# Optimization experiments

Hardware: AMD Instinct MI355X
Metric: run time of the kernel (lower is better)

## Reference

```python
import jax, jax.numpy as jnp
import numpy as np

N, IN_DIM, LAT, NB = 4096, 3000, 64, 2
SINKHORN_ITERS = 3


def _bce_logits(x, y):
    # torch BCEWithLogitsLoss, mean reduction, numerically stable
    return jnp.mean(jnp.maximum(x, 0.0) - x * y + jnp.log1p(jnp.exp(-jnp.abs(x))))


def _forward(feature_set, adj_set, graph_neigh_set, label_CSL_set, dist_mat_set,
             enc_W, dec_W, Ms, disc_W, disc_b, perm_idx):
    nb = feature_set.shape[0]
    hs = []
    loss_sl = 0.0
    loss_feat = 0.0
    for k in range(nb):  # small fixed loop over slices
        x, adj, mask, lab = feature_set[k], adj_set[k], graph_neigh_set[k], label_CSL_set[k]
        h = adj @ (x @ enc_W[k])            # GCN encode: spmm(adj, x @ W)
        out = adj @ (h @ dec_W[k])          # GCN decode
        x_a = x[perm_idx[k]]                # permutation(x): row shuffle
        h_a = adj @ (x_a @ enc_W[k])
        hr, har = jax.nn.relu(h), jax.nn.relu(h_a)

        def readout(emb):
            vsum = mask @ emb
            ge = vsum / mask.sum(1, keepdims=True)
            nrm = jnp.linalg.norm(ge, axis=1, keepdims=True)
            return ge / jnp.maximum(nrm, 1e-12)   # F.normalize p=2

        g = jax.nn.sigmoid(readout(hr))
        g_a = jax.nn.sigmoid(readout(har))

        def disc(c, hp, hm):
            s1 = jnp.einsum('nd,de,ne->n', hp, disc_W, c) + disc_b[0]
            s2 = jnp.einsum('nd,de,ne->n', hm, disc_W, c) + disc_b[0]
            return jnp.stack([s1, s2], axis=1)  # [N,2]

        ret = disc(g, hr, har)
        ret_a = disc(g_a, har, hr)
        loss_sl = loss_sl + _bce_logits(ret, lab) + _bce_logits(ret_a, lab)
        loss_feat = loss_feat + jnp.mean((x - out) ** 2)
        hs.append(h)

    loss_align = 0.0; loss_align_fix = 0.0; loss_maintain = 0.0
    loss_marginal = 0.0; loss_sparsity = 0.0
    for k in range(1, nb):
        src, tgt = hs[k - 1], hs[k]
        M = Ms[k - 1]
        m1, m2 = src.shape[0], tgt.shape[0]
        C = (src @ M) @ (tgt @ M).T / jnp.sqrt(jnp.float32(M.shape[0]))
        P = jax.nn.softmax(C, axis=1) / m1
        # NonSquareSinkhornKnopp.fit: alternate row/col normalization to uniform marginals
        for _ in range(SINKHORN_ITERS):
            P = P / (m1 * P.sum(1, keepdims=True))
            P = P / (m2 * P.sum(0, keepdims=True))
        cxy = P / P.sum(1, keepdims=True)
        cyx = P.T / P.T.sum(1, keepdims=True)
        # cdist(src, tgt)
        d2 = jnp.sum(src ** 2, 1)[:, None] + jnp.sum(tgt ** 2, 1)[None, :] - 2.0 * (src @ tgt.T)
        cd = jnp.sqrt(jnp.maximum(d2, 1e-12))
        loss_align = loss_align + jnp.sum(P * cd)
        f0, f1 = feature_set[k - 1], feature_set[k]
        loss_align_fix = loss_align_fix + jnp.mean((f0 - cxy @ f1) ** 2) + jnp.mean((f1 - cyx @ f0) ** 2)
        D0, D1 = dist_mat_set[k - 1], dist_mat_set[k]
        diff1 = D0 - cxy @ (D1 @ cxy.T)
        diff2 = D1 - cyx @ (D0 @ cyx.T)
        loss_maintain = loss_maintain + jnp.linalg.norm(diff1) / m1 + jnp.linalg.norm(diff2) / m2
        # replicate torch F.kl_div(input, target) = mean(target*(log target - input))
        p = jnp.full((m2,), 1.0 / m2, jnp.float32)
        q = P.sum(0)
        kld_pq = jnp.mean(q * (jnp.log(q) - p))
        kld_pp = jnp.mean(p * (jnp.log(p) - p))
        loss_marginal = loss_marginal + (kld_pq - kld_pp) * m2
        loss_sparsity = loss_sparsity - jnp.sum(P * jnp.log(P + 1e-10))
    return jnp.stack([loss_sl, loss_feat, loss_align, loss_align_fix,
                      loss_maintain, loss_marginal, loss_sparsity])


def setup_inputs():
    key = jax.random.key(0)
    ks = jax.random.split(key, 12)
    feature_set = jax.random.normal(ks[0], (NB, N, IN_DIM), jnp.float32)
    A = jax.random.uniform(ks[1], (NB, N, N), jnp.float32)
    adj_set = A / A.sum(-1, keepdims=True)  # row-stochastic dense stand-in for normalized sparse adj
    mask = (jax.random.uniform(ks[2], (NB, N, N)) < 0.01).astype(jnp.float32)
    graph_neigh_set = mask + jnp.eye(N, dtype=jnp.float32)[None]  # nonzero row sums
    lab = jnp.concatenate([jnp.ones((N, 1)), jnp.zeros((N, 1))], axis=1).astype(jnp.float32)
    label_CSL_set = jnp.broadcast_to(lab, (NB, N, 2))
    D = jax.random.uniform(ks[3], (NB, N, N), jnp.float32)
    dist_mat_set = 0.5 * (D + jnp.swapaxes(D, 1, 2))
    perm_idx = jnp.stack([jax.random.permutation(ks[4 + i], N) for i in range(NB)]).astype(jnp.int32)
    s_enc = np.float32(np.sqrt(2.0 / (IN_DIM + LAT)))
    enc_W = jax.random.normal(ks[6], (NB, IN_DIM, LAT), jnp.float32) * s_enc
    dec_W = jax.random.normal(ks[7], (NB, LAT, IN_DIM), jnp.float32) * s_enc
    s_lat = np.float32(np.sqrt(1.0 / LAT))
    Ms = jax.random.normal(ks[8], (NB - 1, LAT, LAT), jnp.float32) * s_lat
    disc_W = jax.random.normal(ks[9], (LAT, LAT), jnp.float32) * s_lat
    disc_b = jnp.zeros((1,), jnp.float32)
    return dict(feature_set=feature_set, adj_set=adj_set, graph_neigh_set=graph_neigh_set,
                label_CSL_set=label_CSL_set, dist_mat_set=dist_mat_set, perm_idx=perm_idx,
                enc_W=enc_W, dec_W=dec_W, Ms=Ms, disc_W=disc_W, disc_b=disc_b)


def reference(feature_set, adj_set, graph_neigh_set, label_CSL_set, dist_mat_set,
              perm_idx, enc_W, dec_W, Ms, disc_W, disc_b):
    return _forward(feature_set, adj_set, graph_neigh_set, label_CSL_set, dist_mat_set,
                    enc_W, dec_W, Ms, disc_W, disc_b, perm_idx)
```

## Files before the change

kernel.cpp:

```cpp
#include <hip/hip_runtime.h>
#include <cmath>

constexpr int kN   = 4096;
constexpr int kIN  = 3000;
constexpr int kINp = 3072;
constexpr int kLAT = 64;

enum { SL = 0, FEAT, ALN, FXA, FXB, SM1, SM2, SPS, NSLOT };

typedef __bf16 bf16x8 __attribute__((ext_vector_type(8)));
typedef float f32x4 __attribute__((ext_vector_type(4)));
typedef unsigned short u16x8 __attribute__((ext_vector_type(8)));
typedef unsigned short u16x4 __attribute__((ext_vector_type(4)));

template<bool IS_MAX>
__device__ __forceinline__ float blk_red(float v) {
  __shared__ float buf[8];
  #pragma unroll
  for (int s = 32; s > 0; s >>= 1) {
    float o = __shfl_down(v, s, 64);
    v = IS_MAX ? fmaxf(v, o) : (v + o);
  }
  int lane = threadIdx.x & 63, wv = threadIdx.x >> 6, nw = blockDim.x >> 6;
  __syncthreads();
  if (lane == 0) buf[wv] = v;
  __syncthreads();
  float r = buf[0];
  for (int i = 1; i < nw; i++) r = IS_MAX ? fmaxf(r, buf[i]) : (r + buf[i]);
  return r;
}

__device__ __forceinline__ float wave_red_sum(float v) {
  #pragma unroll
  for (int s = 32; s > 0; s >>= 1) v += __shfl_down(v, s, 64);
  return v;
}

__device__ __forceinline__ unsigned short f2bf(float f) {
  unsigned u = __builtin_bit_cast(unsigned, f);
  u += 0x7fffu + ((u >> 16) & 1u);
  return (unsigned short)(u >> 16);
}
__device__ __forceinline__ float bf2f(unsigned short h) {
  return __builtin_bit_cast(float, (unsigned)h << 16);
}

__device__ __forceinline__ void gload16(const unsigned short* g, unsigned short* l) {
  __builtin_amdgcn_global_load_lds(
      (const __attribute__((address_space(1))) unsigned int*)g,
      (__attribute__((address_space(3))) unsigned int*)l, 16, 0, 0);
}

#define VMW(n) asm volatile("s_waitcnt vmcnt(" #n ")" ::: "memory")

template<int EPI, int XBF>
__global__ __launch_bounds__(256)
void bt_mfma_k(const unsigned short* __restrict__ A, const unsigned short* __restrict__ Bt,
               unsigned short* __restrict__ Cb, float* __restrict__ Cf,
               const void* __restrict__ Xv,
               const float* __restrict__ rowdiv, const float* __restrict__ coldiv,
               float* __restrict__ slot, int gx, int Nc, int K, int ldX, int sym)
{
  __shared__ unsigned short AB[3 * 8192];

  int orig = blockIdx.x;
  int bx, by;
  if (EPI == 2 && sym) {
    int x = orig & 7, i = orig >> 3;
    int u = x * 66 + i;
    float disc = 4225.f - 8.f * (float)u;
    by = (int)((65.f - sqrtf(fmaxf(disc, 0.f))) * 0.5f);
    while (by > 0 && 32 * by - by * (by - 1) / 2 > u) by--;
    while (32 * (by + 1) - (by + 1) * by / 2 <= u) by++;
    bx = by + (u - (32 * by - by * (by - 1) / 2));
  } else {
    int x = orig & 7, tt = orig >> 3;
    bx = tt >> 2;
    by = x * 4 + (tt & 3);
  }
  const int row0 = by * 128, col0 = bx * 128;

  const int t = threadIdx.x, l = t & 63, wv = t >> 6;
  const int wr = wv >> 1, wc = wv & 1;
  const int lr = l & 15, lkh = (l >> 4) << 3;

  f32x4 acc[4][4];
  #pragma unroll
  for (int i = 0; i < 4; i++)
    #pragma unroll
    for (int j = 0; j < 4; j++) acc[i][j] = (f32x4){0.f, 0.f, 0.f, 0.f};

  const int srow = l >> 2;
  const int sk   = (l & 3) << 3;
  const unsigned short* Ab = A  + (size_t)(row0 + srow) * K + sk;
  const unsigned short* Bb = Bt + (size_t)(col0 + srow) * K + sk;

  const int NT = K >> 5;

  auto STAGE = [&](int kt, int buf) {
    unsigned short* As = AB + buf * 8192;
    unsigned short* Bs = As + 4096;
    int k0 = kt << 5;
    #pragma unroll
    for (int h2 = 0; h2 < 2; h2++) {
      int c = wv * 2 + h2;
      gload16(Ab + (size_t)c * 16 * K + k0, As + c * 512);
      gload16(Bb + (size_t)c * 16 * K + k0, Bs + c * 512);
    }
  };

  STAGE(0, 0);
  if (NT > 1) STAGE(1, 1);
  if (NT > 2) STAGE(2, 2);
  int cur = 0;

  for (int kt = 0; kt < NT; ++kt) {
    int ahead = NT - 1 - kt;
    if (ahead >= 2)      { VMW(8); }
    else if (ahead == 1) { VMW(4); }
    else                 { VMW(0); }
    __builtin_amdgcn_sched_barrier(0);
    __builtin_amdgcn_s_barrier();

    const unsigned short* As = AB + cur * 8192;
    const unsigned short* Bs = As + 4096;
    u16x8 af[4], bfv[4];
    #pragma unroll
    for (int mi = 0; mi < 4; mi++)
      af[mi] = *(const u16x8*)&As[(wr * 64 + mi * 16 + lr) * 32 + lkh];
    #pragma unroll
    for (int ni = 0; ni < 4; ni++)
      bfv[ni] = *(const u16x8*)&Bs[(wc * 64 + ni * 16 + lr) * 32 + lkh];
    #pragma unroll
    for (int mi = 0; mi < 4; mi++)
      #pragma unroll
      for (int ni = 0; ni < 4; ni++)
        acc[mi][ni] = __builtin_amdgcn_mfma_f32_16x16x32_bf16(
            __builtin_bit_cast(bf16x8, af[mi]),
            __builtin_bit_cast(bf16x8, bfv[ni]), acc[mi][ni], 0, 0, 0);

    __builtin_amdgcn_s_barrier();
    if (kt + 3 < NT) STAGE(kt + 3, cur);
    cur = (cur == 2) ? 0 : cur + 1;
  }

  const int lcol = l & 15, lrow = (l >> 4) << 2;
  if (EPI == 0) {
    #pragma unroll
    for (int mi = 0; mi < 4; mi++) {
      int rr = row0 + wr * 64 + mi * 16 + lrow;
      #pragma unroll
      for (int ni = 0; ni < 4; ni++) {
        int cc = col0 + wc * 64 + ni * 16 + lcol;
        #pragma unroll
        for (int r = 0; r < 4; r++) {
          float v = acc[mi][ni][r];
          if (rowdiv) v /= rowdiv[rr + r];
          Cb[(size_t)(rr + r) * 4096 + cc] = f2bf(v);
        }
      }
    }
  } else if (EPI == 1) {
    #pragma unroll
    for (int mi = 0; mi < 4; mi++) {
      int rr = row0 + wr * 64 + mi * 16 + lrow;
      #pragma unroll
      for (int ni = 0; ni < 4; ni++) {
        int cc = col0 + wc * 64 + ni * 16 + lcol;
        #pragma unroll
        for (int r = 0; r < 4; r++)
          Cf[(size_t)(rr + r) * 4096 + cc] = acc[mi][ni][r];
      }
    }
  } else if (EPI == 2) {
    const float* Xf = (const float*)Xv;
    const unsigned short* Xh = (const unsigned short*)Xv;
    float part = 0.f;
    #pragma unroll
    for (int mi = 0; mi < 4; mi++) {
      int rr = row0 + wr * 64 + mi * 16 + lrow;
      #pragma unroll
      for (int ni = 0; ni < 4; ni++) {
        int cc = col0 + wc * 64 + ni * 16 + lcol;
        if (cc < Nc) {
          float cd = coldiv ? coldiv[cc] : 1.f;
          #pragma unroll
          for (int r = 0; r < 4; r++) {
            float v = acc[mi][ni][r];
            if (rowdiv) v /= rowdiv[rr + r];
            v /= cd;
            size_t xi = (size_t)(rr + r) * ldX + cc;
            float xval = XBF ? bf2f(Xh[xi]) : Xf[xi];
            float d = xval - v;
            part = fmaf(d, d, part);
          }
        }
      }
    }
    part = blk_red<false>(part);
    if (t == 0) {
      float wgt = (sym && col0 > row0) ? 2.f : 1.f;
      atomicAdd(slot, part * wgt);
    }
  } else {
    const unsigned short* Ph = (const unsigned short*)Xv;
    float a = 0.f, sp = 0.f;
    #pragma unroll
    for (int mi = 0; mi < 4; mi++) {
      int rr = row0 + wr * 64 + mi * 16 + lrow;
      #pragma unroll
      for (int ni = 0; ni < 4; ni++) {
        int cc = col0 + wc * 64 + ni * 16 + lcol;
        #pragma unroll
        for (int r = 0; r < 4; r++) {
          float g = acc[mi][ni][r];
          float p = bf2f(Ph[(size_t)(rr + r) * ldX + cc]);
          float d2 = rowdiv[rr + r] + coldiv[cc] - 2.f * g;
          a = fmaf(p, sqrtf(fmaxf(d2, 1e-12f)), a);
          sp = fmaf(p, logf(p + 1e-10f), sp);
        }
      }
    }
    a = blk_red<false>(a);
    sp = blk_red<false>(sp);
    if (t == 0) { atomicAdd(&slot[ALN], a); atomicAdd(&slot[SPS], sp); }
  }
}

__global__ __launch_bounds__(256)
void ns_mfma_k(const unsigned short* __restrict__ A, const unsigned short* __restrict__ Bt,
               float* __restrict__ C, int Nc, int K, int KC, int ldC)
{
  __shared__ unsigned short AB[2 * 8192];
  int ks = blockIdx.x & 15, strip = blockIdx.x >> 4;
  const int row0 = strip * 128;
  const int kbase = ks * KC;

  const int t = threadIdx.x, l = t & 63, wv = t >> 6;
  const int wr = wv >> 1, wc = wv & 1;
  const int lr = l & 15, lkh = (l >> 4) << 3;

  f32x4 acc[4][4];
  #pragma unroll
  for (int i = 0; i < 4; i++)
    #pragma unroll
    for (int j = 0; j < 4; j++) acc[i][j] = (f32x4){0.f, 0.f, 0.f, 0.f};

  const int srow = l >> 2;
  const int sk   = (l & 3) << 3;
  const unsigned short* Ab = A  + (size_t)(row0 + srow) * K + kbase + sk;
  const unsigned short* Bb = Bt + (size_t)srow * K + kbase + sk;

  const int NT = KC >> 5;

  auto STAGE = [&](int kt, int buf) {
    unsigned short* As = AB + buf * 8192;
    unsigned short* Bs = As + 4096;
    int k0 = kt << 5;
    #pragma unroll
    for (int h2 = 0; h2 < 2; h2++) {
      int c = wv * 2 + h2;
      gload16(Ab + (size_t)c * 16 * K + k0, As + c * 512);
      gload16(Bb + (size_t)c * 16 * K + k0, Bs + c * 512);
    }
  };

  STAGE(0, 0);
  if (NT > 1) STAGE(1, 1);
  int cur = 0;

  for (int kt = 0; kt < NT; ++kt) {
    if (kt + 1 < NT) { VMW(4); }
    else             { VMW(0); }
    __builtin_amdgcn_sched_barrier(0);
    __builtin_amdgcn_s_barrier();

    const unsigned short* As = AB + cur * 8192;
    const unsigned short* Bs = As + 4096;
    u16x8 af[4], bfv[4];
    #pragma unroll
    for (int mi = 0; mi < 4; mi++)
      af[mi] = *(const u16x8*)&As[(wr * 64 + mi * 16 + lr) * 32 + lkh];
    #pragma unroll
    for (int ni = 0; ni < 4; ni++)
      bfv[ni] = *(const u16x8*)&Bs[(wc * 64 + ni * 16 + lr) * 32 + lkh];
    #pragma unroll
    for (int mi = 0; mi < 4; mi++)
      #pragma unroll
      for (int ni = 0; ni < 4; ni++)
        acc[mi][ni] = __builtin_amdgcn_mfma_f32_16x16x32_bf16(
            __builtin_bit_cast(bf16x8, af[mi]),
            __builtin_bit_cast(bf16x8, bfv[ni]), acc[mi][ni], 0, 0, 0);

    __builtin_amdgcn_s_barrier();
    if (kt + 2 < NT) STAGE(kt + 2, cur);
    cur ^= 1;
  }

  const int lcol = l & 15, lrow = (l >> 4) << 2;
  #pragma unroll
  for (int mi = 0; mi < 4; mi++) {
    int rr = row0 + wr * 64 + mi * 16 + lrow;
    #pragma unroll
    for (int ni = 0; ni < 4; ni++) {
      int cc = wc * 64 + ni * 16 + lcol;
      if (cc < Nc) {
        #pragma unroll
        for (int r = 0; r < 4; r++)
          atomicAdd(&C[(size_t)(rr + r) * ldC + cc], acc[mi][ni][r]);
      }
    }
  }
}

__global__ void cvt_k(const float* __restrict__ s, unsigned short* __restrict__ d,
                      int n8, float scale)
{
  int i = blockIdx.x * 256 + threadIdx.x;
  if (i < n8) {
    float4 a = ((const float4*)s)[2 * i], b = ((const float4*)s)[2 * i + 1];
    u16x8 w;
    w[0] = f2bf(a.x * scale); w[1] = f2bf(a.y * scale);
    w[2] = f2bf(a.z * scale); w[3] = f2bf(a.w * scale);
    w[4] = f2bf(b.x * scale); w[5] = f2bf(b.y * scale);
    w[6] = f2bf(b.z * scale); w[7] = f2bf(b.w * scale);
    ((u16x8*)d)[i] = w;
  }
}

__global__ void cvt_rs_k(const float* __restrict__ s, unsigned short* __restrict__ d,
                         float* __restrict__ mrs)
{
  int i = blockIdx.x * 256 + threadIdx.x;
  float4 a = ((const float4*)s)[2 * i], b = ((const float4*)s)[2 * i + 1];
  u16x8 w;
  w[0] = f2bf(a.x); w[1] = f2bf(a.y); w[2] = f2bf(a.z); w[3] = f2bf(a.w);
  w[4] = f2bf(b.x); w[5] = f2bf(b.y); w[6] = f2bf(b.z); w[7] = f2bf(b.w);
  ((u16x8*)d)[i] = w;
  float s8 = a.x + a.y + a.z + a.w + b.x + b.y + b.z + b.w;
  float ws = wave_red_sum(s8);
  if ((threadIdx.x & 63) == 0) atomicAdd(&mrs[i >> 9], ws);
}

__global__ void cvt_pad_k(const float* __restrict__ s, unsigned short* __restrict__ d)
{
  int i = blockIdx.x * 256 + threadIdx.x;
  int row = i / 384, c8 = (i - row * 384) * 8;
  u16x8 w = (u16x8)0;
  if (c8 < kIN) {
    const float* sp = s + (size_t)row * kIN + c8;
    float4 a = *(const float4*)sp, b = *(const float4*)(sp + 4);
    w[0] = f2bf(a.x); w[1] = f2bf(a.y); w[2] = f2bf(a.z); w[3] = f2bf(a.w);
    w[4] = f2bf(b.x); w[5] = f2bf(b.y); w[6] = f2bf(b.z); w[7] = f2bf(b.w);
  }
  ((u16x8*)d)[i] = w;
}

__global__ void cvtsq_k(const float* __restrict__ H, unsigned short* __restrict__ hb,
                        float* __restrict__ outv)
{
  int row = blockIdx.x * 4 + (threadIdx.x >> 6), j = threadIdx.x & 63;
  float v = H[(size_t)row * 128 + j];
  hb[(size_t)row * 64 + j] = f2bf(v);
  float p = wave_red_sum(v * v);
  if (j == 0) outv[row] = p;
}

template<bool RELU>
__global__ void tr_k(const float* __restrict__ src, unsigned short* __restrict__ dst,
                     int R, int C, int sld, int dld)
{
  __shared__ float tile[32][33];
  int c0 = blockIdx.x * 32, r0 = blockIdx.y * 32;
  int tr_ = threadIdx.x >> 3, tc4 = (threadIdx.x & 7) << 2;
  #pragma unroll
  for (int j = 0; j < 4; j++) {
    int r = r0 + tr_, c = c0 + tc4 + j;
    float v = (r < R && c < C) ? src[(size_t)r * sld + c] : 0.f;
    if (RELU) v = fmaxf(v, 0.f);
    tile[tr_][tc4 + j] = v;
  }
  __syncthreads();
  u16x4 wv;
  #pragma unroll
  for (int j = 0; j < 4; j++) wv[j] = f2bf(tile[tc4 + j][tr_]);
  *(u16x4*)&dst[(size_t)(c0 + tr_) * dld + r0 + tc4] = wv;
}

__global__ void tr_bf_k(const unsigned short* __restrict__ src,
                        unsigned short* __restrict__ dst, int R, int C)
{
  __shared__ unsigned short tile[32][36];
  int c0 = blockIdx.x * 32, r0 = blockIdx.y * 32;
  int tr_ = threadIdx.x >> 3, tc4 = (threadIdx.x & 7) << 2;
  *(u16x4*)&tile[tr_][tc4] = *(const u16x4*)&src[(size_t)(r0 + tr_) * C + c0 + tc4];
  __syncthreads();
  u16x4 w;
  #pragma unroll
  for (int j = 0; j < 4; j++) w[j] = tile[tc4 + j][tr_];
  *(u16x4*)&dst[(size_t)(c0 + tr_) * R + r0 + tc4] = w;
}

template<bool RELU>
__global__ __launch_bounds__(256)
void gemm_small_k(const float* __restrict__ A, const float* __restrict__ B,
                  float* __restrict__ C, int M, int Nc, int K,
                  int ldA, int ldB, int ldC)
{
  __shared__ float As[16][68];
  __shared__ float Bs[16][68];
  int tid = threadIdx.x;
  int tx = tid & 15, ty = tid >> 4;
  int row0 = blockIdx.y * 64, col0 = blockIdx.x * 64;
  float acc[4][4] = {};

  for (int k0 = 0; k0 < K; k0 += 16) {
    {
      int m = tid >> 2, kk = (tid & 3) << 2;
      const float* ap = A + (size_t)(row0 + m) * ldA + k0 + kk;
      float4 v = *(const float4*)ap;
      if (RELU) {
        v.x = fmaxf(v.x, 0.f); v.y = fmaxf(v.y, 0.f);
        v.z = fmaxf(v.z, 0.f); v.w = fmaxf(v.w, 0.f);
      }
      As[kk + 0][m] = v.x; As[kk + 1][m] = v.y; As[kk + 2][m] = v.z; As[kk + 3][m] = v.w;
    }
    {
      int kk = tid >> 4, c = (tid & 15) << 2;
      const float* bp = B + (size_t)(k0 + kk) * ldB + col0 + c;
      #pragma unroll
      for (int i = 0; i < 4; i++)
        Bs[kk][c + i] = (col0 + c + i < Nc) ? bp[i] : 0.f;
    }
    __syncthreads();
    #pragma unroll
    for (int kk = 0; kk < 16; kk++) {
      float4 a4 = *(const float4*)&As[kk][ty << 2];
      float4 b4 = *(const float4*)&Bs[kk][tx << 2];
      float av[4] = {a4.x, a4.y, a4.z, a4.w};
      float bv[4] = {b4.x, b4.y, b4.z, b4.w};
      #pragma unroll
      for (int i = 0; i < 4; i++)
        #pragma unroll
        for (int j = 0; j < 4; j++)
          acc[i][j] = fmaf(av[i], bv[j], acc[i][j]);
    }
    __syncthreads();
  }
  #pragma unroll
  for (int i = 0; i < 4; i++) {
    int r = row0 + (ty << 2) + i;
    #pragma unroll
    for (int j = 0; j < 4; j++) {
      int c = col0 + (tx << 2) + j;
      if (c < Nc) C[(size_t)r * ldC + c] = acc[i][j];
    }
  }
}

__global__ __launch_bounds__(256)
void sink_k(float* __restrict__ P, unsigned short* __restrict__ Pb,
            const float* __restrict__ cs_in, float* __restrict__ cs_out,
            float* __restrict__ rs, int mode)
{
  int tid = threadIdx.x;
  int r0 = blockIdx.x * 8;
  float csl[16] = {};
  float cdiv[16];
  if (mode != 0) {
    #pragma unroll
    for (int t = 0; t < 4; t++) {
      float4 c4 = ((const float4*)cs_in)[tid + t * 256];
      cdiv[4 * t + 0] = 1.f / (4096.f * c4.x);
      cdiv[4 * t + 1] = 1.f / (4096.f * c4.y);
      cdiv[4 * t + 2] = 1.f / (4096.f * c4.z);
      cdiv[4 * t + 3] = 1.f / (4096.f * c4.w);
    }
  }
  for (int rr = 0; rr < 8; rr++) {
    int row = r0 + rr;
    float4* prow = (float4*)(P + (size_t)row * 4096);
    float4 r[4];
    #pragma unroll
    for (int t = 0; t < 4; t++) r[t] = prow[tid + t * 256];

    if (mode == 0) {
      float m = -3.4e38f;
      #pragma unroll
      for (int t = 0; t < 4; t++)
        m = fmaxf(m, fmaxf(fmaxf(r[t].x, r[t].y), fmaxf(r[t].z, r[t].w)));
      m = blk_red<true>(m);
      float s = 0.f;
      #pragma unroll
      for (int t = 0; t < 4; t++) {
        r[t].x = expf(r[t].x - m); r[t].y = expf(r[t].y - m);
        r[t].z = expf(r[t].z - m); r[t].w = expf(r[t].w - m);
        s += r[t].x + r[t].y + r[t].z + r[t].w;
      }
      s = blk_red<false>(s);
      float f = 1.f / (s * 4096.f);
      #pragma unroll
      for (int t = 0; t < 4; t++) {
        r[t].x *= f; r[t].y *= f; r[t].z *= f; r[t].w *= f;
        prow[tid + t * 256] = r[t];
        csl[4 * t + 0] += r[t].x; csl[4 * t + 1] += r[t].y;
        csl[4 * t + 2] += r[t].z; csl[4 * t + 3] += r[t].w;
      }
    } else {
      float s = 0.f;
      #pragma unroll
      for (int t = 0; t < 4; t++) {
        r[t].x *= cdiv[4 * t + 0]; r[t].y *= cdiv[4 * t + 1];
        r[t].z *= cdiv[4 * t + 2]; r[t].w *= cdiv[4 * t + 3];
        s += r[t].x + r[t].y + r[t].z + r[t].w;
      }
      s = blk_red<false>(s);
      if (mode == 1) {
        float f = 1.f / (4096.f * s);
        #pragma unroll
        for (int t = 0; t < 4; t++) {
          r[t].x *= f; r[t].y *= f; r[t].z *= f; r[t].w *= f;
          prow[tid + t * 256] = r[t];
          csl[4 * t + 0] += r[t].x; csl[4 * t + 1] += r[t].y;
          csl[4 * t + 2] += r[t].z; csl[4 * t + 3] += r[t].w;
        }
      } else {
        if (tid == 0) rs[row] = s;
        #pragma unroll
        for (int t = 0; t < 4; t++) {
          prow[tid + t * 256] = r[t];
          u16x4 w;
          w[0] = f2bf(r[t].x); w[1] = f2bf(r[t].y);
          w[2] = f2bf(r[t].z); w[3] = f2bf(r[t].w);
          *(u16x4*)&Pb[(size_t)row * 4096 + 4 * (tid + t * 256)] = w;
          csl[4 * t + 0] += r[t].x; csl[4 * t + 1] += r[t].y;
          csl[4 * t + 2] += r[t].z; csl[4 * t + 3] += r[t].w;
        }
      }
    }
  }
  #pragma unroll
  for (int t = 0; t < 4; t++) {
    int j = 4 * (tid + t * 256);
    atomicAdd(&cs_out[j + 0], csl[4 * t + 0]);
    atomicAdd(&cs_out[j + 1], csl[4 * t + 1]);
    atomicAdd(&cs_out[j + 2], csl[4 * t + 2]);
    atomicAdd(&cs_out[j + 3], csl[4 * t + 3]);
  }
}

__global__ void gather_k(float* __restrict__ XP, const int* __restrict__ perm)
{
  int gid = blockIdx.x * 256 + threadIdx.x;
  int i = gid >> 6, j = gid & 63;
  XP[(size_t)i * 128 + 64 + j] = XP[(size_t)perm[i] * 128 + j];
}

__global__ void readout_k(const float* __restrict__ vs2, const float* __restrict__ mrs,
                          float* __restrict__ g2)
{
  int q = blockIdx.x, j = threadIdx.x;
  float v = vs2[(size_t)q * 64 + j] / mrs[q >> 1];
  float p = v * v;
  #pragma unroll
  for (int s = 1; s < 64; s <<= 1) p += __shfl_xor(p, s, 64);
  float nrm = sqrtf(p);
  v = v / fmaxf(nrm, 1e-12f);
  g2[(size_t)q * 64 + j] = 1.f / (1.f + expf(-v));
}

__device__ __forceinline__ float bce_term(float x, float y) {
  return fmaxf(x, 0.f) - x * y + log1pf(expf(-fabsf(x)));
}

__global__ void disc_k(const float* __restrict__ G2, const float* __restrict__ W2,
                       const float* __restrict__ lab, const float* __restrict__ bptr,
                       float* __restrict__ acc)
{
  int i = blockIdx.x, j = threadIdx.x;
  float gj  = G2[(size_t)(2 * i) * 64 + j];
  float gaj = G2[(size_t)(2 * i + 1) * 64 + j];
  float hw  = W2[(size_t)(2 * i) * 64 + j];
  float haw = W2[(size_t)(2 * i + 1) * 64 + j];
  float s1 = hw * gj, s2 = haw * gj, s1a = haw * gaj, s2a = hw * gaj;
  #pragma unroll
  for (int s = 1; s < 64; s <<= 1) {
    s1  += __shfl_xor(s1, s, 64);
    s2  += __shfl_xor(s2, s, 64);
    s1a += __shfl_xor(s1a, s, 64);
    s2a += __shfl_xor(s2a, s, 64);
  }
  if (j == 0) {
    float b = bptr[0];
    float y0 = lab[i * 2 + 0], y1 = lab[i * 2 + 1];
    float t = bce_term(s1 + b, y0) + bce_term(s2 + b, y1)
            + bce_term(s1a + b, y0) + bce_term(s2a + b, y1);
    atomicAdd(&acc[SL], t);
  }
}

__global__ __launch_bounds__(256)
void finalize_k(const float* __restrict__ acc, const float* __restrict__ cs,
                float* __restrict__ out)
{
  int tid = threadIdx.x;
  float invm2 = 1.f / (float)kN;
  float t = 0.f;
  for (int j = tid; j < kN; j += 256) {
    float q = cs[j];
    t += q * (logf(q) - invm2);
  }
  t = blk_red<false>(t);
  if (tid == 0) {
    float kld_pq = t * invm2;
    float kld_pp = invm2 * (logf(invm2) - invm2);
    out[0] = acc[SL] / (2.f * (float)kN);
    out[1] = acc[FEAT] / ((float)kN * (float)kIN);
    out[2] = acc[ALN];
    out[3] = (acc[FXA] + acc[FXB]) / ((float)kN * (float)kIN);
    out[4] = sqrtf(acc[SM1]) / (float)kN + sqrtf(acc[SM2]) / (float)kN;
    out[5] = (kld_pq - kld_pp) * (float)kN;
    out[6] = -acc[SPS];
  }
}

extern "C" void kernel_launch(void* const* d_in, const int* in_sizes, int n_in,
                              void* d_out, int out_size, void* d_ws, size_t ws_size,
                              hipStream_t stream)
{
  (void)in_sizes; (void)n_in; (void)out_size; (void)ws_size;
  const float* feat  = (const float*)d_in[0];
  const float* adjs  = (const float*)d_in[1];
  const float* gmask = (const float*)d_in[2];
  const float* labs  = (const float*)d_in[3];
  const float* dists = (const float*)d_in[4];
  const int*   perms = (const int*)d_in[5];
  const float* encW  = (const float*)d_in[6];
  const float* decW  = (const float*)d_in[7];
  const float* MsW   = (const float*)d_in[8];
  const float* discW = (const float*)d_in[9];
  const float* discb = (const float*)d_in[10];
  float* out = (float*)d_out;

  const size_t SZNN = (size_t)kN * kN;

  char* cur = (char*)d_ws;
  auto alloc = [&](size_t bytes) {
    char* p = cur;
    cur += (bytes + 255) & ~(size_t)255;
    return p;
  };
  float* P            = (float*)alloc(SZNN * 4);
  unsigned short* Pb  = (unsigned short*)alloc(SZNN * 2);
  unsigned short* PbT = (unsigned short*)alloc(SZNN * 2);
  unsigned short* Db  = (unsigned short*)alloc(SZNN * 2);
  unsigned short* ajb = (unsigned short*)alloc(SZNN * 2);
  unsigned short* xb0 = (unsigned short*)alloc((size_t)kN * kINp * 2);
  unsigned short* xb1 = (unsigned short*)alloc((size_t)kN * kINp * 2);
  unsigned short* dWtb= (unsigned short*)alloc((size_t)kINp * kLAT * 2);
  unsigned short* ahb = (unsigned short*)alloc((size_t)kN * kLAT * 2);
  unsigned short* encWtp = (unsigned short*)alloc((size_t)128 * kINp * 2);
  unsigned short* XPt = (unsigned short*)alloc((size_t)128 * kN * 2);
  unsigned short* hbTp= (unsigned short*)alloc((size_t)128 * kN * 2);
  unsigned short* HRt = (unsigned short*)alloc((size_t)128 * kN * 2);
  unsigned short* smb = (unsigned short*)alloc((size_t)kN * kLAT * 2);
  unsigned short* tmb = (unsigned short*)alloc((size_t)kN * kLAT * 2);
  unsigned short* h0b = (unsigned short*)alloc((size_t)kN * kLAT * 2);
  unsigned short* h1b = (unsigned short*)alloc((size_t)kN * kLAT * 2);
  float* XP  = (float*)alloc((size_t)kN * 128 * 4);
  float* HH0 = (float*)alloc((size_t)kN * 128 * 4);
  float* HH1 = (float*)alloc((size_t)kN * 128 * 4);
  float* VS  = (float*)alloc((size_t)kN * 128 * 4);
  float* G2  = (float*)alloc((size_t)kN * 128 * 4);
  float* W2  = (float*)alloc((size_t)kN * 128 * 4);
  float* SM_ = (float*)alloc((size_t)kN * kLAT * 4);
  float* TM_ = (float*)alloc((size_t)kN * kLAT * 4);
  float* ah  = (float*)alloc((size_t)kN * kLAT * 4);
  float* sns = (float*)alloc(kN * 4);
  float* snt = (float*)alloc(kN * 4);
  float* rs  = (float*)alloc(kN * 4);
  float* cs  = (float*)alloc(kN * 4);
  float* csA = (float*)alloc(kN * 4);
  float* csB = (float*)alloc(kN * 4);
  float* mrs = (float*)alloc(kN * 4);
  float* acc = (float*)alloc(NSLOT * 4);

  unsigned short* Tb  = (unsigned short*)P;
  unsigned short* ftb = ajb;

  hipMemsetAsync(acc, 0, NSLOT * sizeof(float), stream);

  for (int k = 0; k < 2; k++) {
    const float* x    = feat  + (size_t)k * kN * kIN;
    const float* adj  = adjs  + (size_t)k * SZNN;
    const float* msk  = gmask + (size_t)k * SZNN;
    const float* lab  = labs  + (size_t)k * kN * 2;
    const int*   perm = perms + (size_t)k * kN;
    const float* eW   = encW  + (size_t)k * kIN * kLAT;
    const float* dW   = decW  + (size_t)k * kLAT * kIN;
    float* HHk = (k == 0) ? HH0 : HH1;
    unsigned short* xbk = (k == 0) ? xb0 : xb1;

    cvt_pad_k<<<6144, 256, 0, stream>>>(x, xbk);
    hipMemsetAsync(encWtp, 0, (size_t)128 * kINp * 2, stream);
    tr_k<false><<<dim3(2, (kIN + 31) / 32), 256, 0, stream>>>(eW, encWtp, kIN, kLAT, kLAT, kINp);
    hipMemsetAsync(XP, 0, (size_t)kN * 128 * 4, stream);
    ns_mfma_k<<<512, 256, 0, stream>>>(xbk, encWtp, XP, kLAT, kINp, kINp / 16, 128);
    gather_k<<<kN * 64 / 256, 256, 0, stream>>>(XP, perm);
    tr_k<false><<<dim3(4, 128), 256, 0, stream>>>(XP, XPt, kN, 128, 128, kN);
    cvt_k<<<(int)(SZNN / 8 / 256), 256, 0, stream>>>(adj, ajb, (int)(SZNN / 8), 1.f);
    hipMemsetAsync(HHk, 0, (size_t)kN * 128 * 4, stream);
    ns_mfma_k<<<512, 256, 0, stream>>>(ajb, XPt, HHk, 128, kN, kN / 16, 128);
    hipMemsetAsync(hbTp, 0, (size_t)128 * kN * 2, stream);
    tr_k<false><<<dim3(2, 128), 256, 0, stream>>>(HHk, hbTp, kN, kLAT, 128, kN);
    hipMemsetAsync(ah, 0, (size_t)kN * kLAT * 4, stream);
    ns_mfma_k<<<512, 256, 0, stream>>>(ajb, hbTp, ah, kLAT, kN, kN / 16, kLAT);
    cvt_k<<<128, 256, 0, stream>>>(ah, ahb, kN * kLAT / 8, 1.f);
    tr_k<false><<<dim3(kINp / 32, 2), 256, 0, stream>>>(dW, dWtb, kLAT, kIN, kIN, kLAT);
    bt_mfma_k<2, 1><<<(kINp / 128) * 32, 256, 0, stream>>>(
        ahb, dWtb, nullptr, nullptr, xbk, nullptr, nullptr, &acc[FEAT],
        kINp / 128, kIN, kLAT, kINp, 0);
    tr_k<true><<<dim3(4, 128), 256, 0, stream>>>(HHk, HRt, kN, 128, 128, kN);
    hipMemsetAsync(mrs, 0, kN * 4, stream);
    cvt_rs_k<<<(int)(SZNN / 8 / 256), 256, 0, stream>>>(msk, ajb, mrs);
    hipMemsetAsync(VS, 0, (size_t)kN * 128 * 4, stream);
    ns_mfma_k<<<512, 256, 0, stream>>>(ajb, HRt, VS, 128, kN, kN / 16, 128);
    readout_k<<<2 * kN, 64, 0, stream>>>(VS, mrs, G2);
    gemm_small_k<true><<<dim3(1, 128), 256, 0, stream>>>(HHk, discW, W2, 2 * kN, kLAT,
                                                         kLAT, kLAT, kLAT, kLAT);
    disc_k<<<kN, 64, 0, stream>>>(G2, W2, lab, discb, acc);
  }

  const float* D0 = dists;
  const float* D1 = dists + SZNN;

  gemm_small_k<false><<<dim3(1, 64), 256, 0, stream>>>(HH0, MsW, SM_, kN, kLAT, kLAT,
                                                       128, kLAT, kLAT);
  gemm_small_k<false><<<dim3(1, 64), 256, 0, stream>>>(HH1, MsW, TM_, kN, kLAT, kLAT,
                                                       128, kLAT, kLAT);
  cvt_k<<<128, 256, 0, stream>>>(SM_, smb, kN * kLAT / 8, 0.125f);
  cvt_k<<<128, 256, 0, stream>>>(TM_, tmb, kN * kLAT / 8, 1.f);
  bt_mfma_k<1, 0><<<1024, 256, 0, stream>>>(smb, tmb, nullptr, P, nullptr, nullptr, nullptr,
                                            nullptr, 32, kN, kLAT, 0, 0);

  hipMemsetAsync(csA, 0, kN * 4, stream);
  sink_k<<<512, 256, 0, stream>>>(P, nullptr, nullptr, csA, nullptr, 0);
  hipMemsetAsync(csB, 0, kN * 4, stream);
  sink_k<<<512, 256, 0, stream>>>(P, nullptr, csA, csB, nullptr, 1);
  hipMemsetAsync(csA, 0, kN * 4, stream);
  sink_k<<<512, 256, 0, stream>>>(P, nullptr, csB, csA, nullptr, 1);
  hipMemsetAsync(cs, 0, kN * 4, stream);
  sink_k<<<512, 256, 0, stream>>>(P, Pb, csA, cs, rs, 2);

  tr_k<false><<<dim3(kN / 32, kN / 32), 256, 0, stream>>>(P, PbT, kN, kN, kN, kN);

  cvtsq_k<<<1024, 256, 0, stream>>>(HH0, h0b, sns);
  cvtsq_k<<<1024, 256, 0, stream>>>(HH1, h1b, snt);
  bt_mfma_k<3, 1><<<1024, 256, 0, stream>>>(h0b, h1b, nullptr, nullptr, Pb, sns, snt, acc,
                                            32, kN, kLAT, kN, 0);

  tr_bf_k<<<dim3(kINp / 32, kN / 32), 256, 0, stream>>>(xb1, ftb, kN, kINp);
  bt_mfma_k<2, 1><<<(kINp / 128) * 32, 256, 0, stream>>>(
      Pb, ftb, nullptr, nullptr, xb0, rs, nullptr, &acc[FXA], kINp / 128, kIN, kN, kINp, 0);
  tr_bf_k<<<dim3(kINp / 32, kN / 32), 256, 0, stream>>>(xb0, ftb, kN, kINp);
  bt_mfma_k<2, 1><<<(kINp / 128) * 32, 256, 0, stream>>>(
      PbT, ftb, nullptr, nullptr, xb1, cs, nullptr, &acc[FXB], kINp / 128, kIN, kN, kINp, 0);

  cvt_k<<<(int)(SZNN / 8 / 256), 256, 0, stream>>>(D1, Db, (int)(SZNN / 8), 1.f);
  bt_mfma_k<0, 0><<<1024, 256, 0, stream>>>(Pb, Db, Tb, nullptr, nullptr, rs, nullptr,
                                            nullptr, 32, kN, kN, 0, 0);
  bt_mfma_k<2, 0><<<528, 256, 0, stream>>>(Tb, Pb, nullptr, nullptr, D0, nullptr, rs,
                                           &acc[SM1], 32, kN, kN, kN, 1);
  cvt_k<<<(int)(SZNN / 8 / 256), 256, 0, stream>>>(D0, Db, (int)(SZNN / 8), 1.f);
  bt_mfma_k<0, 0><<<1024, 256, 0, stream>>>(PbT, Db, Tb, nullptr, nullptr, cs, nullptr,
                                            nullptr, 32, kN, kN, 0, 0);
  bt_mfma_k<2, 0><<<528, 256, 0, stream>>>(Tb, PbT, nullptr, nullptr, D1, nullptr, cs,
                                           &acc[SM2], 32, kN, kN, kN, 1);

  finalize_k<<<1, 256, 0, stream>>>(acc, cs, out);
}
```

Before: 1.981 ms.

## Merge paired GEMM+reduction launches into one persistent grid-stride kernel

Adds a bt2_mfma_k kernel that runs the tiles of two independent GEMMs with a squared-error epilogue in one launch, using a grid-stride loop over the combined tile list. The two feature-transport GEMMs and the two symmetric smoothness GEMMs are each merged this way. Separate scratch buffers (ftb2, Tb2) let both operands stay live at once. The goal is to fill the GPU better and cut launch and tail gaps, paid for with extra buffer reuse of ajb/Db and a trailing barrier in blk_red.

```diff
diff --git a/kernel.cpp b/kernel.cpp
--- a/kernel.cpp
+++ b/kernel.cpp
@@ -27,6 +27,7 @@
   __syncthreads();
   float r = buf[0];
   for (int i = 1; i < nw; i++) r = IS_MAX ? fmaxf(r, buf[i]) : (r + buf[i]);
+  __syncthreads();
   return r;
 }
 
@@ -52,6 +53,16 @@
 }
 
 #define VMW(n) asm volatile("s_waitcnt vmcnt(" #n ")" ::: "memory")
+
+__device__ __forceinline__ void tri_decode(int lu, int& bx, int& by) {
+  int x = lu & 7, i = lu >> 3;
+  int u = x * 66 + i;
+  float disc = 4225.f - 8.f * (float)u;
+  by = (int)((65.f - sqrtf(fmaxf(disc, 0.f))) * 0.5f);
+  while (by > 0 && 32 * by - by * (by - 1) / 2 > u) by--;
+  while (32 * (by + 1) - (by + 1) * by / 2 <= u) by++;
+  bx = by + (u - (32 * by - by * (by - 1) / 2));
+}
 
 template<int EPI, int XBF>
 __global__ __launch_bounds__(256)
@@ -59,25 +70,14 @@
                unsigned short* __restrict__ Cb, float* __restrict__ Cf,
                const void* __restrict__ Xv,
                const float* __restrict__ rowdiv, const float* __restrict__ coldiv,
-               float* __restrict__ slot, int gx, int Nc, int K, int ldX, int sym)
+               float* __restrict__ slot, int gx, int Nc, int K, int ldX)
 {
   __shared__ unsigned short AB[3 * 8192];
 
   int orig = blockIdx.x;
-  int bx, by;
-  if (EPI == 2 && sym) {
-    int x = orig & 7, i = orig >> 3;
-    int u = x * 66 + i;
-    float disc = 4225.f - 8.f * (float)u;
-    by = (int)((65.f - sqrtf(fmaxf(disc, 0.f))) * 0.5f);
-    while (by > 0 && 32 * by - by * (by - 1) / 2 > u) by--;
-    while (32 * (by + 1) - (by + 1) * by / 2 <= u) by++;
-    bx = by + (u - (32 * by - by * (by - 1) / 2));
-  } else {
-    int x = orig & 7, tt = orig >> 3;
-    bx = tt >> 2;
-    by = x * 4 + (tt & 3);
-  }
+  int x = orig & 7, tt = orig >> 3;
+  int bx = tt >> 2;
+  int by = x * 4 + (tt & 3);
   const int row0 = by * 128, col0 = bx * 128;
 
   const int t = threadIdx.x, l = t & 63, wv = t >> 6;
@@ -198,10 +198,7 @@
       }
     }
     part = blk_red<false>(part);
-    if (t == 0) {
-      float wgt = (sym && col0 > row0) ? 2.f : 1.f;
-      atomicAdd(slot, part * wgt);
-    }
+    if (t == 0) atomicAdd(slot, part);
   } else {
     const unsigned short* Ph = (const unsigned short*)Xv;
     float a = 0.f, sp = 0.f;
@@ -224,6 +221,134 @@
     a = blk_red<false>(a);
     sp = blk_red<false>(sp);
     if (t == 0) { atomicAdd(&slot[ALN], a); atomicAdd(&slot[SPS], sp); }
+  }
+}
+
+template<int XBF, int SYM>
+__global__ __launch_bounds__(256)
+void bt2_mfma_k(const unsigned short* __restrict__ A0, const unsigned short* __restrict__ B0,
+                const void* __restrict__ X0, const float* __restrict__ rd0,
+                const float* __restrict__ cd0, float* __restrict__ slot0,
+                const unsigned short* __restrict__ A1, const unsigned short* __restrict__ B1,
+                const void* __restrict__ X1, const float* __restrict__ rd1,
+                const float* __restrict__ cd1, float* __restrict__ slot1,
+                int gx, int Nc, int K, int ldX, int ntiles, int split)
+{
+  __shared__ unsigned short AB[3 * 8192];
+  const int t = threadIdx.x, l = t & 63, wv = t >> 6;
+  const int wr = wv >> 1, wc = wv & 1;
+  const int lr = l & 15, lkh = (l >> 4) << 3;
+  const int srow = l >> 2;
+  const int sk   = (l & 3) << 3;
+  const int NT = K >> 5;
+
+  for (int u = blockIdx.x; u < ntiles; u += gridDim.x) {
+    const int s1 = (u >= split);
+    const int lu = s1 ? (u - split) : u;
+    const unsigned short* A  = s1 ? A1 : A0;
+    const unsigned short* Bt = s1 ? B1 : B0;
+    const void* Xv           = s1 ? X1 : X0;
+    const float* rowdiv      = s1 ? rd1 : rd0;
+    const float* coldiv      = s1 ? cd1 : cd0;
+    float* slot              = s1 ? slot1 : slot0;
+
+    int bx, by;
+    if (SYM) {
+      tri_decode(lu, bx, by);
+    } else {
+      int x = lu & 7, tt = lu >> 3;
+      bx = tt >> 2;
+      by = x * 4 + (tt & 3);
+    }
+    const int row0 = by * 128, col0 = bx * 128;
+
+    f32x4 acc[4][4];
+    #pragma unroll
+    for (int i = 0; i < 4; i++)
+      #pragma unroll
+      for (int j = 0; j < 4; j++) acc[i][j] = (f32x4){0.f, 0.f, 0.f, 0.f};
+
+    const unsigned short* Ab = A  + (size_t)(row0 + srow) * K + sk;
+    const unsigned short* Bb = Bt + (size_t)(col0 + srow) * K + sk;
+
+    auto STAGE = [&](int kt, int buf) {
+      unsigned short* As = AB + buf * 8192;
+      unsigned short* Bs = As + 4096;
+      int k0 = kt << 5;
+      #pragma unroll
+      for (int h2 = 0; h2 < 2; h2++) {
+        int c = wv * 2 + h2;
+        gload16(Ab + (size_t)c * 16 * K + k0, As + c * 512);
+        gload16(Bb + (size_t)c * 16 * K + k0, Bs + c * 512);
+      }
+    };
+
+    STAGE(0, 0);
+    if (NT > 1) STAGE(1, 1);
+    if (NT > 2) STAGE(2, 2);
+    int cur = 0;
+
+    for (int kt = 0; kt < NT; ++kt) {
+      int ahead = NT - 1 - kt;
+      if (ahead >= 2)      { VMW(8); }
+      else if (ahead == 1) { VMW(4); }
+      else                 { VMW(0); }
+      __builtin_amdgcn_sched_barrier(0);
+      __builtin_amdgcn_s_barrier();
+
+      const unsigned short* As = AB + cur * 8192;
+      const unsigned short* Bs = As + 4096;
+      u16x8 af[4], bfv[4];
+      #pragma unroll
+      for (int mi = 0; mi < 4; mi++)
+        af[mi] = *(const u16x8*)&As[(wr * 64 + mi * 16 + lr) * 32 + lkh];
+      #pragma unroll
+      for (int ni = 0; ni < 4; ni++)
+        bfv[ni] = *(const u16x8*)&Bs[(wc * 64 + ni * 16 + lr) * 32 + lkh];
+      #pragma unroll
+      for (int mi = 0; mi < 4; mi++)
+        #pragma unroll
+        for (int ni = 0; ni < 4; ni++)
+          acc[mi][ni] = __builtin_amdgcn_mfma_f32_16x16x32_bf16(
+              __builtin_bit_cast(bf16x8, af[mi]),
+              __builtin_bit_cast(bf16x8, bfv[ni]), acc[mi][ni], 0, 0, 0);
+
+      __builtin_amdgcn_s_barrier();
+      if (kt + 3 < NT) STAGE(kt + 3, cur);
+      cur = (cur == 2) ? 0 : cur + 1;
+    }
+
+    const int lcol = l & 15, lrow = (l >> 4) << 2;
+    const float* Xf = (const float*)Xv;
+    const unsigned short* Xh = (const unsigned short*)Xv;
+    float part = 0.f;
+    #pragma unroll
+    for (int mi = 0; mi < 4; mi++) {
+      int rr = row0 + wr * 64 + mi * 16 + lrow;
+      #pragma unroll
+      for (int ni = 0; ni < 4; ni++) {
+        int cc = col0 + wc * 64 + ni * 16 + lcol;
+        if (cc < Nc) {
+          float cd = coldiv ? coldiv[cc] : 1.f;
+          #pragma unroll
+          for (int r = 0; r < 4; r++) {
+            float v = acc[mi][ni][r];
+            if (rowdiv) v /= rowdiv[rr + r];
+            v /= cd;
+            size_t xi = (size_t)(rr + r) * ldX + cc;
+            float xval = XBF ? bf2f(Xh[xi]) : Xf[xi];
+            float d = xval - v;
+            part = fmaf(d, d, part);
+          }
+        }
+      }
+    }
+    part = blk_red<false>(part);
+    if (t == 0) {
+      float wgt = (SYM && col0 > row0) ? 2.f : 1.f;
+      atomicAdd(slot, part * wgt);
+    }
+    __syncthreads();
   }
 }
 
@@ -685,8 +810,10 @@
   float* mrs = (float*)alloc(kN * 4);
   float* acc = (float*)alloc(NSLOT * 4);
 
-  unsigned short* Tb  = (unsigned short*)P;
+  unsigned short* Tb1 = (unsigned short*)P;
   unsigned short* ftb = ajb;
+  unsigned short* ftb2= Db;
+  unsigned short* Tb2 = ajb;
 
   hipMemsetAsync(acc, 0, NSLOT * sizeof(float), stream);
 
@@ -719,7 +846,7 @@
     tr_k<false><<<dim3(kINp / 32, 2), 256, 0, stream>>>(dW, dWtb, kLAT, kIN, kIN, kLAT);
     bt_mfma_k<2, 1><<<(kINp / 128) * 32, 256, 0, stream>>>(
         ahb, dWtb, nullptr, nullptr, xbk, nullptr, nullptr, &acc[FEAT],
-        kINp / 128, kIN, kLAT, kINp, 0);
+        kINp / 128, kIN, kLAT, kINp);
     tr_k<true><<<dim3(4, 128), 256, 0, stream>>>(HHk, HRt, kN, 128, 128, kN);
     hipMemsetAsync(mrs, 0, kN * 4, stream);
     cvt_rs_k<<<(int)(SZNN / 8 / 256), 256, 0, stream>>>(msk, ajb, mrs);
@@ -741,7 +868,7 @@
   cvt_k<<<128, 256, 0, stream>>>(SM_, smb, kN * kLAT / 8, 0.125f);
   cvt_k<<<128, 256, 0, stream>>>(TM_, tmb, kN * kLAT / 8, 1.f);
   bt_mfma_k<1, 0><<<1024, 256, 0, stream>>>(smb, tmb, nullptr, P, nullptr, nullptr, nullptr,
-                                            nullptr, 32, kN, kLAT, 0, 0);
+                                            nullptr, 32, kN, kLAT, 0);
 
   hipMemsetAsync(csA, 0, kN * 4, stream);
   sink_k<<<512, 256, 0, stream>>>(P, nullptr, nullptr, csA, nullptr, 0);
@@ -757,25 +884,25 @@
   cvtsq_k<<<1024, 256, 0, stream>>>(HH0, h0b, sns);
   cvtsq_k<<<1024, 256, 0, stream>>>(HH1, h1b, snt);
   bt_mfma_k<3, 1><<<1024, 256, 0, stream>>>(h0b, h1b, nullptr, nullptr, Pb, sns, snt, acc,
-                                            32, kN, kLAT, kN, 0);
+                                            32, kN, kLAT, kN);
 
   tr_bf_k<<<dim3(kINp / 32, kN / 32), 256, 0, stream>>>(xb1, ftb, kN, kINp);
-  bt_mfma_k<2, 1><<<(kINp / 128) * 32, 256, 0, stream>>>(
-      Pb, ftb, nullptr, nullptr, xb0, rs, nullptr, &acc[FXA], kINp / 128, kIN, kN, kINp, 0);
-  tr_bf_k<<<dim3(kINp / 32, kN / 32), 256, 0, stream>>>(xb0, ftb, kN, kINp);
-  bt_mfma_k<2, 1><<<(kINp / 128) * 32, 256, 0, stream>>>(
-      PbT, ftb, nullptr, nullptr, xb1, cs, nullptr, &acc[FXB], kINp / 128, kIN, kN, kINp, 0);
+  tr_bf_k<<<dim3(kINp / 32, kN / 32), 256, 0, stream>>>(xb0, ftb2, kN, kINp);
+  bt2_mfma_k<1, 0><<<1024, 256, 0, stream>>>(
+      Pb,  ftb,  xb0, rs, nullptr, &acc[FXA],
+      PbT, ftb2, xb1, cs, nullptr, &acc[FXB],
+      kINp / 128, kIN, kN, kINp, 2 * (kINp / 128) * 32, (kINp / 128) * 32);
 
   cvt_k<<<(int)(SZNN / 8 / 256), 256, 0, stream>>>(D1, Db, (int)(SZNN / 8), 1.f);
-  bt_mfma_k<0, 0><<<1024, 256, 0, stream>>>(Pb, Db, Tb, nullptr, nullptr, rs, nullptr,
-                                            nullptr, 32, kN, kN, 0, 0);
-  bt_mfma_k<2, 0><<<528, 256, 0, stream>>>(Tb, Pb, nullptr, nullptr, D0, nullptr, rs,
-                                           &acc[SM1], 32, kN, kN, kN, 1);
+  bt_mfma_k<0, 0><<<1024, 256, 0, stream>>>(Pb, Db, Tb1, nullptr, nullptr, rs, nullptr,
+                                            nullptr, 32, kN, kN, 0);
   cvt_k<<<(int)(SZNN / 8 / 256), 256, 0, stream>>>(D0, Db, (int)(SZNN / 8), 1.f);
-  bt_mfma_k<0, 0><<<1024, 256, 0, stream>>>(PbT, Db, Tb, nullptr, nullptr, cs, nullptr,
-                                            nullptr, 32, kN, kN, 0, 0);
-  bt_mfma_k<2, 0><<<528, 256, 0, stream>>>(Tb, PbT, nullptr, nullptr, D1, nullptr, cs,
-                                           &acc[SM2], 32, kN, kN, kN, 1);
+  bt_mfma_k<0, 0><<<1024, 256, 0, stream>>>(PbT, Db, Tb2, nullptr, nullptr, cs, nullptr,
+                                            nullptr, 32, kN, kN, 0);
+  bt2_mfma_k<0, 1><<<1024, 256, 0, stream>>>(
+      Tb1, Pb,  D0, nullptr, rs, &acc[SM1],
+      Tb2, PbT, D1, nullptr, cs, &acc[SM2],
+      32, kN, kN, kN, 1056, 528);
 
   finalize_k<<<1, 256, 0, stream>>>(acc, cs, out);
 }
```

Result: slower. 2.132 ms (+7.6%).
